# Performance work log

Measured on AMD Instinct MI355X. Metric: run time of the kernel, lower is better.

The kernel has to match this reference:

```python
import jax, jax.numpy as jnp
import numpy as np

NUM_STEPS = 151
STEP = 2.0 / (NUM_STEPS - 1)
TSIZE = NUM_STEPS  # t = -1, -1+step, ..., 1
N = 4096
D = 512
NUM_CLASSES = 100


def setup_inputs() -> dict:
    key = jax.random.key(0)
    k1, k2 = jax.random.split(key)
    feats = jax.random.normal(k1, (N, D), dtype=jnp.float32)
    # L2-normalize so pairwise dot products lie in [-1, 1] (histogram support)
    feats = feats / jnp.linalg.norm(feats, axis=1, keepdims=True)
    classes = jax.random.randint(k2, (N,), 0, NUM_CLASSES, dtype=jnp.int64)
    return {"features": feats, "classes": classes}


def reference(features, classes):
    n = features.shape[0]
    # pairwise cosine similarities, upper triangle (i < j)
    dists = features @ features.T  # [N, N]
    iu, ju = jnp.triu_indices(n, k=1)  # static index arrays
    s = dists[iu, ju]                  # [P] similarities
    pos = classes[iu] == classes[ju]   # [P] same-class mask

    # triangular soft-binning exactly as in the torch code:
    # f = floor(s/step)*step; bin at t==f gets (s-f)/step, bin at t==f+step gets (f+step-s)/step
    f = jnp.floor(s / STEP) * STEP
    j = jnp.floor(s / STEP).astype(jnp.int32) + (NUM_STEPS - 1) // 2  # index of t == f
    wa = (s - f) / STEP
    wb = (f + STEP - s) / STEP
    va = (j >= 0) & (j < TSIZE)
    vb = (j + 1 >= 0) & (j + 1 < TSIZE)
    ja = jnp.clip(j, 0, TSIZE - 1)
    jb = jnp.clip(j + 1, 0, TSIZE - 1)

    def hist(mask, size):
        w_a = jnp.where(va & mask, wa, 0.0)
        w_b = jnp.where(vb & mask, wb, 0.0)
        h = jnp.zeros(TSIZE, s.dtype).at[ja].add(w_a).at[jb].add(w_b)
        return h / size.astype(s.dtype)

    pos_size = pos.sum()
    neg_size = (~pos).sum()
    hist_pos = hist(pos, pos_size)
    hist_neg = hist(~pos, neg_size)
    # tril-masked repeat + sum(0) == inclusive cumulative sum of hist_pos
    hist_pos_cdf = jnp.cumsum(hist_pos)
    loss = jnp.sum(hist_neg * hist_pos_cdf)
    return loss
```

## Files before the change

kernel.cpp:

```cpp
#include <hip/hip_runtime.h>


#define N_PTS   4096
#define DIM     512
#define TSIZE   151
#define HALF_T  75
#define BM      128
#define NTILES  32
#define NBLOCKS 528
#define P_TOTAL 8386560u
#define STEPF   (2.0f / 150.0f)
#define STEPINV 75.0f
#define NCOPY   16
#define HSTRIDE 309

typedef short bfrag __attribute__((ext_vector_type(8)));
typedef float ffrag __attribute__((ext_vector_type(4)));
typedef unsigned short u16;
typedef unsigned int   u32;

__device__ __forceinline__ ffrag mfma16(bfrag a, bfrag b, ffrag c) {
  return __builtin_amdgcn_mfma_f32_16x16x32_bf16(a, b, c, 0, 0, 0);
}

__device__ __forceinline__ void split4(float4 v, uint2* hi, uint2* lo) {
  u32 u0 = __float_as_uint(v.x), u1 = __float_as_uint(v.y);
  u32 u2 = __float_as_uint(v.z), u3 = __float_as_uint(v.w);
  float r0 = v.x - __uint_as_float(u0 & 0xFFFF0000u);
  float r1 = v.y - __uint_as_float(u1 & 0xFFFF0000u);
  float r2 = v.z - __uint_as_float(u2 & 0xFFFF0000u);
  float r3 = v.w - __uint_as_float(u3 & 0xFFFF0000u);
  hi->x = (u0 >> 16) | (u1 & 0xFFFF0000u);
  hi->y = (u2 >> 16) | (u3 & 0xFFFF0000u);
  lo->x = (__float_as_uint(r0) >> 16) | (__float_as_uint(r1) & 0xFFFF0000u);
  lo->y = (__float_as_uint(r2) >> 16) | (__float_as_uint(r3) & 0xFFFF0000u);
}

__device__ __forceinline__ void bin_epilogue(
    const ffrag (&acc)[4][4], float* h, const int* clsA, const int* clsB,
    int wy, int wx, int l4, int l16, bool diag, u32* myPos)
{
  #pragma unroll
  for (int fi = 0; fi < 4; ++fi) {
    #pragma unroll
    for (int fj = 0; fj < 4; ++fj) {
      #pragma unroll
      for (int r = 0; r < 4; ++r) {
        int li = wy * 64 + fi * 16 + l4 * 4 + r;
        int lj = wx * 64 + fj * 16 + l16;
        if (diag && li >= lj) continue;
        float s  = acc[fi][fj][r];
        float jf = floorf(s * STEPINV);
        int   jb = (int)jf + HALF_T;
        float f  = jf * STEPF;
        float wa = (s - f) * STEPINV;
        float wb = (f + STEPF - s) * STEPINV;
        bool  pos = (clsA[li] == clsB[lj]);
        *myPos += pos ? 1u : 0u;
        int off = pos ? 0 : TSIZE;
        if (jb >= 0 && jb < TSIZE)         unsafeAtomicAdd(h + off + jb, wa);
        if (jb + 1 >= 0 && jb + 1 < TSIZE) unsafeAtomicAdd(h + off + jb + 1, wb);
      }
    }
  }
}

__device__ __forceinline__ void tile_decode(int orig, int* bi_, int* bj_) {
  int sbid = (orig & 7) * 66 + (orig >> 3);
  int rem = sbid, cnt = NTILES, bi = 0;
  while (rem >= cnt) { rem -= cnt; --cnt; ++bi; }
  *bi_ = bi; *bj_ = bi + rem;
}

__global__ __launch_bounds__(256) void presplit(
    const float* __restrict__ F, u16* __restrict__ FhiP, u16* __restrict__ FloP,
    float* __restrict__ g_hist, u32* __restrict__ g_pos)
{
  int u = blockIdx.x * 256 + threadIdx.x;
  int row = u >> 6, kb = u & 63;
  const float* src = F + (size_t)row * DIM + kb * 8;
  float4 v0 = *(const float4*)(src);
  float4 v1 = *(const float4*)(src + 4);
  uint2 h0, l0, h1, l1;
  split4(v0, &h0, &l0);
  split4(v1, &h1, &l1);
  uint4 hv; hv.x = h0.x; hv.y = h0.y; hv.z = h1.x; hv.w = h1.y;
  uint4 lv; lv.x = l0.x; lv.y = l0.y; lv.z = l1.x; lv.w = l1.y;
  size_t dst = ((size_t)kb * N_PTS + row) * 8;
  *(uint4*)(FhiP + dst) = hv;
  *(uint4*)(FloP + dst) = lv;
  if (blockIdx.x == 0) {
    for (int i = threadIdx.x; i < 2 * TSIZE; i += 256) g_hist[i] = 0.0f;
    if (threadIdx.x == 0) *g_pos = 0u;
  }
}

__global__ __launch_bounds__(256, 2) void hist_mfma(
    const u16* __restrict__ FhiP, const u16* __restrict__ FloP,
    const int* __restrict__ cls,
    float* __restrict__ g_hist, u32* __restrict__ g_pos)
{
  __shared__ float hist[NCOPY * HSTRIDE];
  __shared__ int clsA[BM], clsB[BM];
  __shared__ u32 posCount;

  const int t = threadIdx.x;
  int bi, bj;
  tile_decode((int)blockIdx.x, &bi, &bj);
  const int rowA = bi * BM, rowB = bj * BM;

  for (int i = t; i < NCOPY * HSTRIDE; i += 256) hist[i] = 0.0f;
  if (t < BM) clsA[t] = cls[rowA + t];
  else        clsB[t - BM] = cls[rowB + (t - BM)];
  if (t == 0) posCount = 0u;

  const int lane = t & 63, w = t >> 6;
  const int wy = w >> 1, wx = w & 1;
  const int l4 = lane >> 4, l16 = lane & 15;

  ffrag acc[4][4] = {};

  const size_t SSTR = (size_t)4 * N_PTS * 8;
  const size_t lb   = (size_t)l4 * N_PTS * 8;
  const size_t ao   = lb + (size_t)(rowA + wy * 64 + l16) * 8;
  const size_t bo   = lb + (size_t)(rowB + wx * 64 + l16) * 8;
  const u16* pAh = FhiP + ao;
  const u16* pAl = FloP + ao;
  const u16* pBh = FhiP + bo;
  const u16* pBl = FloP + bo;

#define LOADF(ah, al, bh, bl, P)                                   \
  do {                                                             \
    _Pragma("unroll") for (int f = 0; f < 4; ++f) {                \
      ah[f] = *(const bfrag*)(pAh + (P) * SSTR + f * 128);         \
      al[f] = *(const bfrag*)(pAl + (P) * SSTR + f * 128);         \
      bh[f] = *(const bfrag*)(pBh + (P) * SSTR + f * 128);         \
      bl[f] = *(const bfrag*)(pBl + (P) * SSTR + f * 128);         \
    }                                                              \
  } while (0)

#define COMPUTE(ah, al, bh, bl)                                    \
  do {                                                             \
    _Pragma("unroll") for (int fj = 0; fj < 4; ++fj)               \
      _Pragma("unroll") for (int fi = 0; fi < 4; ++fi) {           \
        acc[fi][fj] = mfma16(ah[fi], bh[fj], acc[fi][fj]);         \
        acc[fi][fj] = mfma16(al[fi], bh[fj], acc[fi][fj]);         \
        acc[fi][fj] = mfma16(ah[fi], bl[fj], acc[fi][fj]);         \
      }                                                            \
  } while (0)

  bfrag a0h[4], a0l[4], b0h[4], b0l[4];
  bfrag a1h[4], a1l[4], b1h[4], b1l[4];

  LOADF(a0h, a0l, b0h, b0l, 0);
  #pragma unroll 1
  for (int s = 0; s < 7; ++s) {
    LOADF(a1h, a1l, b1h, b1l, 1);
    COMPUTE(a0h, a0l, b0h, b0l);
    LOADF(a0h, a0l, b0h, b0l, 2);
    COMPUTE(a1h, a1l, b1h, b1l);
    pAh += 2 * SSTR; pAl += 2 * SSTR; pBh += 2 * SSTR; pBl += 2 * SSTR;
  }
  LOADF(a1h, a1l, b1h, b1l, 1);
  COMPUTE(a0h, a0l, b0h, b0l);
  COMPUTE(a1h, a1l, b1h, b1l);

#undef LOADF
#undef COMPUTE

  __syncthreads();
  u32 myPos = 0;
  float* h = hist + l16 * HSTRIDE;
  bin_epilogue(acc, h, clsA, clsB, wy, wx, l4, l16, bi == bj, &myPos);
  atomicAdd(&posCount, myPos);
  __syncthreads();

  for (int i = t; i < 2 * TSIZE; i += 256) {
    float v = 0.0f;
    #pragma unroll
    for (int c = 0; c < NCOPY; ++c) v += hist[c * HSTRIDE + i];
    unsafeAtomicAdd(g_hist + i, v);
  }
  if (t == 0) atomicAdd(g_pos, posCount);
}

__global__ __launch_bounds__(256) void finalize(
    const float* __restrict__ g_hist,
    const u32* __restrict__ g_pos,
    float* __restrict__ out)
{
  __shared__ float hp[TSIZE];
  __shared__ float hn[TSIZE];
  __shared__ float red[4];
  const int t = threadIdx.x;
  const float Np = (float)(*g_pos);
  const float Nn = (float)(P_TOTAL - *g_pos);
  if (t < TSIZE) {
    hp[t] = g_hist[t] / Np;
    hn[t] = g_hist[TSIZE + t] / Nn;
  }
  __syncthreads();
  for (int off = 1; off < TSIZE; off <<= 1) {
    float v = 0.0f;
    if (t < TSIZE && t >= off) v = hp[t - off];
    __syncthreads();
    if (t < TSIZE) hp[t] += v;
    __syncthreads();
  }
  float term = (t < TSIZE) ? hn[t] * hp[t] : 0.0f;
  #pragma unroll
  for (int o = 32; o > 0; o >>= 1) term += __shfl_down(term, o);
  if ((t & 63) == 0) red[t >> 6] = term;
  __syncthreads();
  if (t == 0) *out = red[0] + red[1] + red[2] + red[3];
}

extern "C" void kernel_launch(void* const* d_in, const int* in_sizes, int n_in,
                              void* d_out, int out_size, void* d_ws, size_t ws_size,
                              hipStream_t stream) {
  const float* F   = (const float*)d_in[0];
  const int*   cls = (const int*)d_in[1];
  float* g_hist = (float*)d_ws;
  u32*   g_pos  = (u32*)((char*)d_ws + 2 * TSIZE * sizeof(float));
  float* out = (float*)d_out;

  const size_t offH   = 65536;
  u16* FhiP = (u16*)((char*)d_ws + offH);
  u16* FloP = (u16*)((char*)d_ws + offH + (size_t)N_PTS * DIM * sizeof(u16));

  presplit<<<(N_PTS * 64) / 256, 256, 0, stream>>>(F, FhiP, FloP, g_hist, g_pos);
  hist_mfma<<<NBLOCKS, 256, 0, stream>>>(FhiP, FloP, cls, g_hist, g_pos);
  finalize<<<1, 256, 0, stream>>>(g_hist, g_pos, out);
}
```

Measured before the change: 215.3 us.

## Stage bf16 split operands through swizzled LDS with direct global-to-LDS loads

The split bf16 hi/lo operands are now stored row-major. The GEMM stages 128x64 A/B tiles into double-buffered, XOR-swizzled shared memory using global_load_lds, and runs the three split products as 24 sequential K-steps (hi*hi, lo*hi, hi*lo). Before, each wave loaded its fragments straight from global memory in a k-major packed layout. The aim is to share operand tiles across waves and cut redundant global traffic. The histogram copy count is halved to make room for the extra LDS, which may raise atomic contention and lower occupancy.

```diff
diff --git a/kernel.cpp b/kernel.cpp
--- a/kernel.cpp
+++ b/kernel.cpp
@@ -6,12 +6,14 @@
 #define TSIZE   151
 #define HALF_T  75
 #define BM      128
+#define BK      64
+#define NSTEP   24
 #define NTILES  32
 #define NBLOCKS 528
 #define P_TOTAL 8386560u
 #define STEPF   (2.0f / 150.0f)
 #define STEPINV 75.0f
-#define NCOPY   16
+#define NCOPY   8
 #define HSTRIDE 309
 
 typedef short bfrag __attribute__((ext_vector_type(8)));
@@ -34,6 +36,63 @@
   hi->y = (u2 >> 16) | (u3 & 0xFFFF0000u);
   lo->x = (__float_as_uint(r0) >> 16) | (__float_as_uint(r1) & 0xFFFF0000u);
   lo->y = (__float_as_uint(r2) >> 16) | (__float_as_uint(r3) & 0xFFFF0000u);
+}
+
+__device__ __forceinline__ void tile_decode(int orig, int* bi_, int* bj_) {
+  int sbid = (orig & 7) * 66 + (orig >> 3);
+  int rem = sbid, cnt = NTILES, bi = 0;
+  while (rem >= cnt) { rem -= cnt; --cnt; ++bi; }
+  *bi_ = bi; *bj_ = bi + rem;
+}
+
+__device__ __forceinline__ void stage_step(
+    int s, u16* Ad, u16* Bd,
+    const u16* __restrict__ Fhi, const u16* __restrict__ Flo,
+    int rowA, int rowB, int w, int rseg, int swzk)
+{
+  const int region = s >> 3;
+  const int k0 = (s & 7) * BK;
+  const u16* ap = (region == 1) ? Flo : Fhi;
+  const u16* bp = (region == 2) ? Flo : Fhi;
+  #pragma unroll
+  for (int g = 0; g < 4; ++g) {
+    int seg = w * 4 + g;
+    int row = seg * 8 + rseg;
+    size_t ga = (size_t)(rowA + row) * DIM + k0 + swzk;
+    size_t gb = (size_t)(rowB + row) * DIM + k0 + swzk;
+    __builtin_amdgcn_global_load_lds(
+        (const __attribute__((address_space(1))) unsigned int*)(ap + ga),
+        (__attribute__((address_space(3))) unsigned int*)(Ad + seg * 512),
+        16, 0, 0);
+    __builtin_amdgcn_global_load_lds(
+        (const __attribute__((address_space(1))) unsigned int*)(bp + gb),
+        (__attribute__((address_space(3))) unsigned int*)(Bd + seg * 512),
+        16, 0, 0);
+  }
+}
+
+__device__ __forceinline__ void compute_step(
+    const u16* As, const u16* Bs, ffrag (&acc)[4][4],
+    int wy, int wx, int l4, int l16)
+{
+  const int swz = (l16 & 7) << 3;
+  #pragma unroll
+  for (int ks = 0; ks < 2; ++ks) {
+    bfrag a[4], b[4];
+    #pragma unroll
+    for (int f = 0; f < 4; ++f) {
+      int ra = wy * 64 + f * 16 + l16;
+      int rb = wx * 64 + f * 16 + l16;
+      int ko = (ks * 32 + l4 * 8) ^ swz;
+      a[f] = *(const bfrag*)(As + ra * BK + ko);
+      b[f] = *(const bfrag*)(Bs + rb * BK + ko);
+    }
+    #pragma unroll
+    for (int fj = 0; fj < 4; ++fj)
+      #pragma unroll
+      for (int fi = 0; fi < 4; ++fi)
+        acc[fi][fj] = mfma16(a[fi], b[fj], acc[fi][fj]);
+  }
 }
 
 __device__ __forceinline__ void bin_epilogue(
@@ -65,15 +124,8 @@
   }
 }
 
-__device__ __forceinline__ void tile_decode(int orig, int* bi_, int* bj_) {
-  int sbid = (orig & 7) * 66 + (orig >> 3);
-  int rem = sbid, cnt = NTILES, bi = 0;
-  while (rem >= cnt) { rem -= cnt; --cnt; ++bi; }
-  *bi_ = bi; *bj_ = bi + rem;
-}
-
 __global__ __launch_bounds__(256) void presplit(
-    const float* __restrict__ F, u16* __restrict__ FhiP, u16* __restrict__ FloP,
+    const float* __restrict__ F, u16* __restrict__ Fhi, u16* __restrict__ Flo,
     float* __restrict__ g_hist, u32* __restrict__ g_pos)
 {
   int u = blockIdx.x * 256 + threadIdx.x;
@@ -86,9 +138,9 @@
   split4(v1, &h1, &l1);
   uint4 hv; hv.x = h0.x; hv.y = h0.y; hv.z = h1.x; hv.w = h1.y;
   uint4 lv; lv.x = l0.x; lv.y = l0.y; lv.z = l1.x; lv.w = l1.y;
-  size_t dst = ((size_t)kb * N_PTS + row) * 8;
-  *(uint4*)(FhiP + dst) = hv;
-  *(uint4*)(FloP + dst) = lv;
+  size_t dst = (size_t)row * DIM + kb * 8;
+  *(uint4*)(Fhi + dst) = hv;
+  *(uint4*)(Flo + dst) = lv;
   if (blockIdx.x == 0) {
     for (int i = threadIdx.x; i < 2 * TSIZE; i += 256) g_hist[i] = 0.0f;
     if (threadIdx.x == 0) *g_pos = 0u;
@@ -96,10 +148,14 @@
 }
 
 __global__ __launch_bounds__(256, 2) void hist_mfma(
-    const u16* __restrict__ FhiP, const u16* __restrict__ FloP,
+    const u16* __restrict__ Fhi, const u16* __restrict__ Flo,
     const int* __restrict__ cls,
     float* __restrict__ g_hist, u32* __restrict__ g_pos)
 {
+  __shared__ __align__(16) u16 As0[BM * BK];
+  __shared__ __align__(16) u16 As1[BM * BK];
+  __shared__ __align__(16) u16 Bs0[BM * BK];
+  __shared__ __align__(16) u16 Bs1[BM * BK];
   __shared__ float hist[NCOPY * HSTRIDE];
   __shared__ int clsA[BM], clsB[BM];
   __shared__ u32 posCount;
@@ -117,60 +173,27 @@
   const int lane = t & 63, w = t >> 6;
   const int wy = w >> 1, wx = w & 1;
   const int l4 = lane >> 4, l16 = lane & 15;
+  const int rseg = lane >> 3;
+  const int swzk = ((lane & 7) ^ (lane >> 3)) << 3;
 
   ffrag acc[4][4] = {};
 
-  const size_t SSTR = (size_t)4 * N_PTS * 8;
-  const size_t lb   = (size_t)l4 * N_PTS * 8;
-  const size_t ao   = lb + (size_t)(rowA + wy * 64 + l16) * 8;
-  const size_t bo   = lb + (size_t)(rowB + wx * 64 + l16) * 8;
-  const u16* pAh = FhiP + ao;
-  const u16* pAl = FloP + ao;
-  const u16* pBh = FhiP + bo;
-  const u16* pBl = FloP + bo;
-
-#define LOADF(ah, al, bh, bl, P)                                   \
-  do {                                                             \
-    _Pragma("unroll") for (int f = 0; f < 4; ++f) {                \
-      ah[f] = *(const bfrag*)(pAh + (P) * SSTR + f * 128);         \
-      al[f] = *(const bfrag*)(pAl + (P) * SSTR + f * 128);         \
-      bh[f] = *(const bfrag*)(pBh + (P) * SSTR + f * 128);         \
-      bl[f] = *(const bfrag*)(pBl + (P) * SSTR + f * 128);         \
-    }                                                              \
-  } while (0)
-
-#define COMPUTE(ah, al, bh, bl)                                    \
-  do {                                                             \
-    _Pragma("unroll") for (int fj = 0; fj < 4; ++fj)               \
-      _Pragma("unroll") for (int fi = 0; fi < 4; ++fi) {           \
-        acc[fi][fj] = mfma16(ah[fi], bh[fj], acc[fi][fj]);         \
-        acc[fi][fj] = mfma16(al[fi], bh[fj], acc[fi][fj]);         \
-        acc[fi][fj] = mfma16(ah[fi], bl[fj], acc[fi][fj]);         \
-      }                                                            \
-  } while (0)
-
-  bfrag a0h[4], a0l[4], b0h[4], b0l[4];
-  bfrag a1h[4], a1l[4], b1h[4], b1l[4];
-
-  LOADF(a0h, a0l, b0h, b0l, 0);
+  stage_step(0, As0, Bs0, Fhi, Flo, rowA, rowB, w, rseg, swzk);
+  __syncthreads();
+
   #pragma unroll 1
-  for (int s = 0; s < 7; ++s) {
-    LOADF(a1h, a1l, b1h, b1l, 1);
-    COMPUTE(a0h, a0l, b0h, b0l);
-    LOADF(a0h, a0l, b0h, b0l, 2);
-    COMPUTE(a1h, a1l, b1h, b1l);
-    pAh += 2 * SSTR; pAl += 2 * SSTR; pBh += 2 * SSTR; pBl += 2 * SSTR;
-  }
-  LOADF(a1h, a1l, b1h, b1l, 1);
-  COMPUTE(a0h, a0l, b0h, b0l);
-  COMPUTE(a1h, a1l, b1h, b1l);
-
-#undef LOADF
-#undef COMPUTE
-
-  __syncthreads();
+  for (int s2 = 0; s2 < NSTEP / 2; ++s2) {
+    const int s = s2 * 2;
+    if (s + 1 < NSTEP) stage_step(s + 1, As1, Bs1, Fhi, Flo, rowA, rowB, w, rseg, swzk);
+    compute_step(As0, Bs0, acc, wy, wx, l4, l16);
+    __syncthreads();
+    if (s + 2 < NSTEP) stage_step(s + 2, As0, Bs0, Fhi, Flo, rowA, rowB, w, rseg, swzk);
+    compute_step(As1, Bs1, acc, wy, wx, l4, l16);
+    __syncthreads();
+  }
+
   u32 myPos = 0;
-  float* h = hist + l16 * HSTRIDE;
+  float* h = hist + (lane & 7) * HSTRIDE;
   bin_epilogue(acc, h, clsA, clsB, wy, wx, l4, l16, bi == bj, &myPos);
   atomicAdd(&posCount, myPos);
   __syncthreads();
@@ -224,11 +247,11 @@
   u32*   g_pos  = (u32*)((char*)d_ws + 2 * TSIZE * sizeof(float));
   float* out = (float*)d_out;
 
-  const size_t offH   = 65536;
-  u16* FhiP = (u16*)((char*)d_ws + offH);
-  u16* FloP = (u16*)((char*)d_ws + offH + (size_t)N_PTS * DIM * sizeof(u16));
-
-  presplit<<<(N_PTS * 64) / 256, 256, 0, stream>>>(F, FhiP, FloP, g_hist, g_pos);
-  hist_mfma<<<NBLOCKS, 256, 0, stream>>>(FhiP, FloP, cls, g_hist, g_pos);
+  const size_t offH = 65536;
+  u16* Fhi = (u16*)((char*)d_ws + offH);
+  u16* Flo = (u16*)((char*)d_ws + offH + (size_t)N_PTS * DIM * sizeof(u16));
+
+  presplit<<<(N_PTS * 64) / 256, 256, 0, stream>>>(F, Fhi, Flo, g_hist, g_pos);
+  hist_mfma<<<NBLOCKS, 256, 0, stream>>>(Fhi, Flo, cls, g_hist, g_pos);
   finalize<<<1, 256, 0, stream>>>(g_hist, g_pos, out);
 }
```

Result: slower. 234.5 us (+8.9%).
